# Optimization experiments

Hardware: AMD Instinct MI355X
Metric: run time of the kernel (lower is better)

Reference implementation:

```python
import jax, jax.numpy as jnp
import numpy as np

D_MODEL = 768
NUM_HEADS = 12
D_K = D_MODEL // NUM_HEADS


def setup_inputs() -> dict:
    key = jax.random.key(0)
    ks = jax.random.split(key, 12)
    B, S = 4, 2048
    s = 1.0 / np.sqrt(D_MODEL)
    inp = {
        "query": jax.random.normal(ks[0], (B, S, D_MODEL), jnp.float32),
        "key": jax.random.normal(ks[1], (B, S, D_MODEL), jnp.float32),
        "value": jax.random.normal(ks[2], (B, S, D_MODEL), jnp.float32),
        "Wq": jax.random.normal(ks[3], (D_MODEL, D_MODEL), jnp.float32) * s,
        "bq": jnp.zeros((D_MODEL,), jnp.float32),
        "Wk": jax.random.normal(ks[4], (D_MODEL, D_MODEL), jnp.float32) * s,
        "bk": jnp.zeros((D_MODEL,), jnp.float32),
        "Wv": jax.random.normal(ks[5], (D_MODEL, D_MODEL), jnp.float32) * s,
        "bv": jnp.zeros((D_MODEL,), jnp.float32),
        "Wo": jax.random.normal(ks[6], (D_MODEL, D_MODEL), jnp.float32) * s,
        "bo": jnp.zeros((D_MODEL,), jnp.float32),
    }
    return inp


def _split_heads(x):
    B, S, _ = x.shape
    return x.reshape(B, S, NUM_HEADS, D_K).transpose(0, 2, 1, 3)  # [B,H,S,Dk]


def reference(query, key, value, Wq, bq, Wk, bk, Wv, bv, Wo, bo):
    # Linear projections (torch nn.Linear: x @ W.T + b)
    Q = _split_heads(query @ Wq.T + bq)
    K = _split_heads(key @ Wk.T + bk)
    V = _split_heads(value @ Wv.T + bv)
    scale = 1.0 / jnp.sqrt(jnp.asarray(D_K, Q.dtype))
    scores = jnp.einsum("bhqd,bhkd->bhqk", Q, K) * scale  # [B,H,S,S]
    attn = jax.nn.softmax(scores, axis=-1)
    # dropout is identity in eval mode
    out = jnp.einsum("bhqk,bhkd->bhqd", attn, V)  # [B,H,S,Dk]
    B, H, S, Dk = out.shape
    out = out.transpose(0, 2, 1, 3).reshape(B, S, H * Dk)
    return out @ Wo.T + bo
```

## Files before the change

### kernel.cpp

```cpp
#include <hip/hip_runtime.h>
#include <hip/hip_bf16.h>

typedef _Float16 half8 __attribute__((ext_vector_type(8)));
typedef _Float16 h4 __attribute__((ext_vector_type(4)));
typedef __fp16 fp16x2 __attribute__((ext_vector_type(2)));
typedef float f32x4 __attribute__((ext_vector_type(4)));

#define D_MODEL 768
#define NUM_HEADS 12
#define D_K 64
#define SEQ 2048
#define BATCH 4
#define M_TOTAL (BATCH * SEQ)
#define W_ELEMS (D_MODEL * D_MODEL)
#define X_ELEMS (M_TOTAL * D_MODEL)
#define QSCALE 0.18033688011112042f
#define SOFF 4.0f

__device__ __forceinline__ void gll16(const _Float16* g, _Float16* l) {
    __builtin_amdgcn_global_load_lds(
        (const __attribute__((address_space(1))) unsigned int*)g,
        (__attribute__((address_space(3))) unsigned int*)l,
        16, 0, 0);
}

__device__ __forceinline__ void pk2(float a, float b, _Float16* out) {
    fp16x2 r = __builtin_amdgcn_cvt_pkrtz(a, b);
    out[0] = (_Float16)r[0];
    out[1] = (_Float16)r[1];
}

__global__ void convert_all(
    const float* __restrict__ w0, const float* __restrict__ w1,
    const float* __restrict__ w2, const float* __restrict__ w3,
    const float* __restrict__ x0, const float* __restrict__ x1,
    const float* __restrict__ x2, _Float16* __restrict__ dst)
{
    const size_t W4 = W_ELEMS / 4, X4 = X_ELEMS / 4;
    size_t i = (size_t)blockIdx.x * blockDim.x + threadIdx.x;
    const float* src;
    size_t off;
    if (i < 4 * W4) {
        size_t slab = i / W4;
        off = i - slab * W4;
        src = (slab == 0) ? w0 : (slab == 1) ? w1 : (slab == 2) ? w2 : w3;
    } else {
        size_t j = i - 4 * W4;
        size_t slab = j / X4;
        off = j - slab * X4;
        src = (slab == 0) ? x0 : (slab == 1) ? x1 : x2;
    }
    float4 f = ((const float4*)src)[off];
    h4 h;
    h[0] = (_Float16)f.x; h[1] = (_Float16)f.y;
    h[2] = (_Float16)f.z; h[3] = (_Float16)f.w;
    ((h4*)dst)[i] = h;
}

__global__ __launch_bounds__(256) void gemm_qkv(
    const _Float16* __restrict__ Xall, const _Float16* __restrict__ Wall,
    const float* __restrict__ bq, const float* __restrict__ bk, const float* __restrict__ bv,
    _Float16* __restrict__ Qo, _Float16* __restrict__ Ko, _Float16* __restrict__ Vto)
{
    __shared__ __align__(16) char smem[36864];
    _Float16* As = (_Float16*)smem;
    _Float16* Bs = As + 128 * 64;

    const int z = blockIdx.z;
    const _Float16* X = Xall + (size_t)z * X_ELEMS;
    const _Float16* W = Wall + (size_t)z * W_ELEMS;

    const int t = threadIdx.x;
    const int w = t >> 6;
    const int l = t & 63;
    const int ln = t & 15;
    const int quad = (t >> 4) & 3;
    const int wm = w >> 1, wn = w & 1;
    const int m0 = blockIdx.x * 128, n0 = blockIdx.y * 128;

    const int srow = l >> 3;
    const int scol = (l & 7) ^ srow;

    f32x4 acc[4][4] = {};

    for (int k0 = 0; k0 < D_MODEL; k0 += 64) {
#pragma unroll
        for (int jj = 0; jj < 4; ++jj) {
            int j = w * 4 + jj;
            int row = j * 8 + srow;
            gll16(X + (size_t)(m0 + row) * D_MODEL + k0 + scol * 8, As + j * 512);
            gll16(W + (size_t)(n0 + row) * D_MODEL + k0 + scol * 8, Bs + j * 512);
        }
        __syncthreads();

#pragma unroll
        for (int kk = 0; kk < 2; ++kk) {
            half8 a[4], b[4];
#pragma unroll
            for (int i = 0; i < 4; ++i) {
                int ra = wm * 64 + i * 16 + ln;
                int rb = wn * 64 + i * 16 + ln;
                a[i] = *(const half8*)&As[ra * 64 + (((kk * 4 + quad) ^ (ln & 7)) * 8)];
                b[i] = *(const half8*)&Bs[rb * 64 + (((kk * 4 + quad) ^ (ln & 7)) * 8)];
            }
            if (z <= 1) {
#pragma unroll
                for (int i = 0; i < 4; ++i)
#pragma unroll
                    for (int j2 = 0; j2 < 4; ++j2)
                        acc[i][j2] = __builtin_amdgcn_mfma_f32_16x16x32_f16(b[j2], a[i], acc[i][j2], 0, 0, 0);
            } else {
#pragma unroll
                for (int i = 0; i < 4; ++i)
#pragma unroll
                    for (int j2 = 0; j2 < 4; ++j2)
                        acc[i][j2] = __builtin_amdgcn_mfma_f32_16x16x32_f16(a[i], b[j2], acc[i][j2], 0, 0, 0);
            }
        }
        __syncthreads();
    }

    if (z <= 1) {
        const float* bias = (z == 0) ? bq : bk;
        _Float16* dst = (z == 0) ? Qo : Ko;
        const int head = (n0 + wn * 64) >> 6;
#pragma unroll
        for (int i = 0; i < 4; ++i) {
            int m = m0 + wm * 64 + i * 16 + ln;
            int b_ = m >> 11, s_ = m & 2047;
            _Float16* rowp = dst + ((size_t)((b_ * NUM_HEADS + head) * SEQ + s_)) * D_K;
#pragma unroll
            for (int j = 0; j < 4; ++j) {
                int dbase = j * 16 + quad * 4;
                f32x4 bn = *(const f32x4*)&bias[n0 + wn * 64 + dbase];
                h4 o;
#pragma unroll
                for (int r = 0; r < 4; ++r) {
                    float v = acc[i][j][r] + bn[r];
                    if (z == 0) v *= QSCALE;
                    o[r] = (_Float16)v;
                }
                *(h4*)&rowp[dbase] = o;
            }
        }
    } else {
        const float* bias = bv;
        _Float16* T = (_Float16*)smem + (size_t)w * (64 * 72);
#pragma unroll
        for (int i = 0; i < 4; ++i) {
#pragma unroll
            for (int j = 0; j < 4; ++j) {
                float bn = bias[n0 + wn * 64 + j * 16 + ln];
                h4 hh;
#pragma unroll
                for (int r = 0; r < 4; ++r) hh[r] = (_Float16)(acc[i][j][r] + bn);
                *(h4*)&T[(j * 16 + ln) * 72 + i * 16 + quad * 4] = hh;
            }
        }
        const int b_ = m0 >> 11;
        const int s0 = (m0 & 2047) + wm * 64;
        const int head = (n0 >> 6) + wn;
        _Float16* base = Vto + (size_t)(b_ * NUM_HEADS + head) * D_K * SEQ + s0;
#pragma unroll
        for (int r8 = 0; r8 < 8; ++r8) {
            int nl = r8 * 8 + (l >> 3);
            half8 v = *(const half8*)&T[nl * 72 + (l & 7) * 8];
            *(half8*)(base + (size_t)nl * SEQ + (l & 7) * 8) = v;
        }
    }
}

__global__ __launch_bounds__(256) void attn(
    const _Float16* __restrict__ Qg, const _Float16* __restrict__ Kg,
    const _Float16* __restrict__ Vtg, _Float16* __restrict__ ctx)
{
    __shared__ __align__(16) _Float16 Ks[2][64 * 64];
    __shared__ __align__(16) _Float16 Vs[2][64 * 64];

    const int t = threadIdx.x;
    const int w = t >> 6;
    const int l = t & 63;
    const int ln = t & 15;
    const int quad = (t >> 4) & 3;

    const int lid = blockIdx.x + (int)gridDim.x * blockIdx.y;
    const int nid = (lid & 7) * ((SEQ / 128) * (BATCH * NUM_HEADS) / 8) + (lid >> 3);
    const int bh = nid >> 4;
    const int q0 = (nid & 15) * 128 + w * 32;

    const _Float16* Qh = Qg + (size_t)bh * SEQ * D_K;
    const _Float16* Kh = Kg + (size_t)bh * SEQ * D_K;
    const _Float16* Vh = Vtg + (size_t)bh * D_K * SEQ;

    const int srow = l >> 3;
    const int scol = (l & 7) ^ srow;
    const int j0 = w * 2, j1 = w * 2 + 1;
    const _Float16* Ksrc0 = Kh + (size_t)(j0 * 8 + srow) * D_K + scol * 8;
    const _Float16* Ksrc1 = Kh + (size_t)(j1 * 8 + srow) * D_K + scol * 8;
    const _Float16* Vsrc0 = Vh + (size_t)(j0 * 8 + srow) * SEQ + scol * 8;
    const _Float16* Vsrc1 = Vh + (size_t)(j1 * 8 + srow) * SEQ + scol * 8;

    half8 qf[2][2];
#pragma unroll
    for (int qt = 0; qt < 2; ++qt)
#pragma unroll
        for (int dh = 0; dh < 2; ++dh)
            qf[qt][dh] = *(const half8*)(Qh + (size_t)(q0 + qt * 16 + ln) * D_K + dh * 32 + quad * 8);

    f32x4 acc[2][4] = {};
    f32x4 lsum[2] = {};

    gll16(Ksrc0, &Ks[0][j0 * 512]);
    gll16(Ksrc1, &Ks[0][j1 * 512]);
    gll16(Vsrc0, &Vs[0][j0 * 512]);
    gll16(Vsrc1, &Vs[0][j1 * 512]);
    asm volatile("s_waitcnt vmcnt(0)" ::: "memory");
    __builtin_amdgcn_s_barrier();

    int cur = 0;
    for (int c = 0; c < SEQ / 64; ++c) {
        if (c + 1 < SEQ / 64) {
            const size_t koff = (size_t)(c + 1) * 64 * D_K;
            const size_t voff = (size_t)(c + 1) * 64;
            gll16(Ksrc0 + koff, &Ks[cur ^ 1][j0 * 512]);
            gll16(Ksrc1 + koff, &Ks[cur ^ 1][j1 * 512]);
            gll16(Vsrc0 + voff, &Vs[cur ^ 1][j0 * 512]);
            gll16(Vsrc1 + voff, &Vs[cur ^ 1][j1 * 512]);
        }

        const _Float16* Ksc = Ks[cur];
        const _Float16* Vsc = Vs[cur];

        h4 vfr[4][4];
#pragma unroll
        for (int dt = 0; dt < 4; ++dt)
#pragma unroll
            for (int kt = 0; kt < 4; ++kt) {
                int g = kt * 2 + (quad >> 1);
                vfr[dt][kt] = *(const h4*)&Vsc[(dt * 16 + ln) * 64 + ((g ^ (ln & 7)) * 8) + (quad & 1) * 4];
            }

        h4 pB[2][4];
#pragma unroll
        for (int kt = 0; kt < 4; ++kt) {
            half8 kf0 = *(const half8*)&Ksc[(kt * 16 + ln) * 64 + ((quad ^ (ln & 7)) * 8)];
            half8 kf1 = *(const half8*)&Ksc[(kt * 16 + ln) * 64 + (((4 + quad) ^ (ln & 7)) * 8)];
#pragma unroll
            for (int qt = 0; qt < 2; ++qt) {
                f32x4 s = {-SOFF, -SOFF, -SOFF, -SOFF};
                s = __builtin_amdgcn_mfma_f32_16x16x32_f16(kf0, qf[qt][0], s, 0, 0, 0);
                s = __builtin_amdgcn_mfma_f32_16x16x32_f16(kf1, qf[qt][1], s, 0, 0, 0);
                f32x4 p;
                p[0] = __builtin_amdgcn_exp2f(s[0]);
                p[1] = __builtin_amdgcn_exp2f(s[1]);
                p[2] = __builtin_amdgcn_exp2f(s[2]);
                p[3] = __builtin_amdgcn_exp2f(s[3]);
                lsum[qt] += p;
                h4 h;
                pk2(p[0], p[1], (_Float16*)&h);
                pk2(p[2], p[3], ((_Float16*)&h) + 2);
                pB[qt][kt] = h;
            }
        }

#pragma unroll
        for (int dt = 0; dt < 4; ++dt)
#pragma unroll
            for (int kt = 0; kt < 4; ++kt) {
                acc[0][dt] = __builtin_amdgcn_mfma_f32_16x16x16f16(vfr[dt][kt], pB[0][kt], acc[0][dt], 0, 0, 0);
                acc[1][dt] = __builtin_amdgcn_mfma_f32_16x16x16f16(vfr[dt][kt], pB[1][kt], acc[1][dt], 0, 0, 0);
            }

        asm volatile("s_waitcnt vmcnt(0)" ::: "memory");
        __builtin_amdgcn_s_barrier();
        cur ^= 1;
    }

    const int h = bh % NUM_HEADS, b = bh / NUM_HEADS;
#pragma unroll
    for (int qt = 0; qt < 2; ++qt) {
        float lp = lsum[qt][0] + lsum[qt][1] + lsum[qt][2] + lsum[qt][3];
        lp += __shfl_xor(lp, 16);
        lp += __shfl_xor(lp, 32);
        float rinv = __builtin_amdgcn_rcpf(lp);
        int q = q0 + qt * 16 + ln;
#pragma unroll
        for (int dt = 0; dt < 4; ++dt) {
            h4 o;
            o[0] = (_Float16)(acc[qt][dt][0] * rinv);
            o[1] = (_Float16)(acc[qt][dt][1] * rinv);
            o[2] = (_Float16)(acc[qt][dt][2] * rinv);
            o[3] = (_Float16)(acc[qt][dt][3] * rinv);
            *(h4*)&ctx[((size_t)(b * SEQ + q)) * D_MODEL + h * D_K + dt * 16 + quad * 4] = o;
        }
    }
}

__global__ __launch_bounds__(256) void gemm_out(
    const _Float16* __restrict__ A, const _Float16* __restrict__ W,
    const float* __restrict__ bo, float* __restrict__ out)
{
    __shared__ __align__(16) _Float16 As[128 * 64];
    __shared__ __align__(16) _Float16 Bs[128 * 64];

    const int t = threadIdx.x;
    const int w = t >> 6;
    const int l = t & 63;
    const int ln = t & 15;
    const int quad = (t >> 4) & 3;
    const int wm = w >> 1, wn = w & 1;
    const int m0 = blockIdx.x * 128, n0 = blockIdx.y * 128;

    const int srow = l >> 3;
    const int scol = (l & 7) ^ srow;

    f32x4 acc[4][4] = {};

    for (int k0 = 0; k0 < D_MODEL; k0 += 64) {
#pragma unroll
        for (int jj = 0; jj < 4; ++jj) {
            int j = w * 4 + jj;
            int row = j * 8 + srow;
            gll16(A + (size_t)(m0 + row) * D_MODEL + k0 + scol * 8, As + j * 512);
            gll16(W + (size_t)(n0 + row) * D_MODEL + k0 + scol * 8, Bs + j * 512);
        }
        __syncthreads();

#pragma unroll
        for (int kk = 0; kk < 2; ++kk) {
            half8 a[4], b[4];
#pragma unroll
            for (int i = 0; i < 4; ++i) {
                int ra = wm * 64 + i * 16 + ln;
                int rb = wn * 64 + i * 16 + ln;
                a[i] = *(const half8*)&As[ra * 64 + (((kk * 4 + quad) ^ (ln & 7)) * 8)];
                b[i] = *(const half8*)&Bs[rb * 64 + (((kk * 4 + quad) ^ (ln & 7)) * 8)];
            }
#pragma unroll
            for (int i = 0; i < 4; ++i)
#pragma unroll
                for (int j2 = 0; j2 < 4; ++j2)
                    acc[i][j2] = __builtin_amdgcn_mfma_f32_16x16x32_f16(b[j2], a[i], acc[i][j2], 0, 0, 0);
        }
        __syncthreads();
    }

#pragma unroll
    for (int i = 0; i < 4; ++i) {
        int m = m0 + wm * 64 + i * 16 + ln;
        float* rowp = out + (size_t)m * D_MODEL;
#pragma unroll
        for (int j = 0; j < 4; ++j) {
            int nb = n0 + wn * 64 + j * 16 + quad * 4;
            f32x4 o = acc[i][j] + *(const f32x4*)&bo[nb];
            *(f32x4*)&rowp[nb] = o;
        }
    }
}

extern "C" void kernel_launch(void* const* d_in, const int* in_sizes, int n_in,
                              void* d_out, int out_size, void* d_ws, size_t ws_size,
                              hipStream_t stream) {
    const float* query = (const float*)d_in[0];
    const float* key   = (const float*)d_in[1];
    const float* value = (const float*)d_in[2];
    const float* Wq = (const float*)d_in[3];
    const float* bq = (const float*)d_in[4];
    const float* Wk = (const float*)d_in[5];
    const float* bk = (const float*)d_in[6];
    const float* Wv = (const float*)d_in[7];
    const float* bv = (const float*)d_in[8];
    const float* Wo = (const float*)d_in[9];
    const float* bo = (const float*)d_in[10];
    float* out = (float*)d_out;

    _Float16* ws = (_Float16*)d_ws;
    _Float16* Wb  = ws;
    _Float16* Xb  = Wb + 4 * (size_t)W_ELEMS;
    _Float16* Qb  = Xb + 3 * (size_t)X_ELEMS;
    _Float16* Kb  = Qb + (size_t)X_ELEMS;
    _Float16* Vtb = Kb + (size_t)X_ELEMS;
    _Float16* ctx = Vtb + (size_t)X_ELEMS;

    const size_t total4 = (4 * (size_t)W_ELEMS + 3 * (size_t)X_ELEMS) / 4;
    convert_all<<<(int)(total4 / 256), 256, 0, stream>>>(
        Wq, Wk, Wv, Wo, query, key, value, Wb);

    gemm_qkv<<<dim3(M_TOTAL / 128, D_MODEL / 128, 3), 256, 0, stream>>>(
        Xb, Wb, bq, bk, bv, Qb, Kb, Vtb);

    attn<<<dim3(SEQ / 128, BATCH * NUM_HEADS), 256, 0, stream>>>(Qb, Kb, Vtb, ctx);

    gemm_out<<<dim3(M_TOTAL / 128, D_MODEL / 128), 256, 0, stream>>>(
        ctx, Wb + 3 * (size_t)W_ELEMS, bo, out);
}
```

Before: 283.9 us.

## Split attention work across 8 waves with 16 query rows each

The attention block grows from 4 to 8 waves (512 threads), and each wave now owns 16 query rows instead of 32, which halves the per-wave Q fragments, accumulators and P tiles. Each wave loads one 8-row slice of the K/V tiles instead of two, so the cooperative load is spread over twice as many waves. V fragments are now loaded per dt inside the PV loop rather than all up front, and that loop raises wave priority with s_setprio. The aim is lower register pressure, higher occupancy and better latency hiding. In exchange, every wave reads K and V from LDS for only 16 rows, which doubles LDS read traffic per output, and there are more waves per barrier.

```diff
diff --git a/kernel.cpp b/kernel.cpp
--- a/kernel.cpp
+++ b/kernel.cpp
@@ -170,7 +170,7 @@
     }
 }
 
-__global__ __launch_bounds__(256) void attn(
+__global__ __launch_bounds__(512, 6) void attn(
     const _Float16* __restrict__ Qg, const _Float16* __restrict__ Kg,
     const _Float16* __restrict__ Vtg, _Float16* __restrict__ ctx)
 {
@@ -186,7 +186,7 @@
     const int lid = blockIdx.x + (int)gridDim.x * blockIdx.y;
     const int nid = (lid & 7) * ((SEQ / 128) * (BATCH * NUM_HEADS) / 8) + (lid >> 3);
     const int bh = nid >> 4;
-    const int q0 = (nid & 15) * 128 + w * 32;
+    const int q0 = (nid & 15) * 128 + w * 16;
 
     const _Float16* Qh = Qg + (size_t)bh * SEQ * D_K;
     const _Float16* Kh = Kg + (size_t)bh * SEQ * D_K;
@@ -194,82 +194,66 @@
 
     const int srow = l >> 3;
     const int scol = (l & 7) ^ srow;
-    const int j0 = w * 2, j1 = w * 2 + 1;
-    const _Float16* Ksrc0 = Kh + (size_t)(j0 * 8 + srow) * D_K + scol * 8;
-    const _Float16* Ksrc1 = Kh + (size_t)(j1 * 8 + srow) * D_K + scol * 8;
-    const _Float16* Vsrc0 = Vh + (size_t)(j0 * 8 + srow) * SEQ + scol * 8;
-    const _Float16* Vsrc1 = Vh + (size_t)(j1 * 8 + srow) * SEQ + scol * 8;
-
-    half8 qf[2][2];
-#pragma unroll
-    for (int qt = 0; qt < 2; ++qt)
-#pragma unroll
-        for (int dh = 0; dh < 2; ++dh)
-            qf[qt][dh] = *(const half8*)(Qh + (size_t)(q0 + qt * 16 + ln) * D_K + dh * 32 + quad * 8);
-
-    f32x4 acc[2][4] = {};
-    f32x4 lsum[2] = {};
-
-    gll16(Ksrc0, &Ks[0][j0 * 512]);
-    gll16(Ksrc1, &Ks[0][j1 * 512]);
-    gll16(Vsrc0, &Vs[0][j0 * 512]);
-    gll16(Vsrc1, &Vs[0][j1 * 512]);
+    const _Float16* Ksrc = Kh + (size_t)(w * 8 + srow) * D_K + scol * 8;
+    const _Float16* Vsrc = Vh + (size_t)(w * 8 + srow) * SEQ + scol * 8;
+
+    half8 qf[2];
+#pragma unroll
+    for (int dh = 0; dh < 2; ++dh)
+        qf[dh] = *(const half8*)(Qh + (size_t)(q0 + ln) * D_K + dh * 32 + quad * 8);
+
+    f32x4 acc[4] = {};
+    f32x4 lsum = {};
+
+    gll16(Ksrc, &Ks[0][w * 512]);
+    gll16(Vsrc, &Vs[0][w * 512]);
     asm volatile("s_waitcnt vmcnt(0)" ::: "memory");
     __builtin_amdgcn_s_barrier();
 
     int cur = 0;
     for (int c = 0; c < SEQ / 64; ++c) {
         if (c + 1 < SEQ / 64) {
-            const size_t koff = (size_t)(c + 1) * 64 * D_K;
-            const size_t voff = (size_t)(c + 1) * 64;
-            gll16(Ksrc0 + koff, &Ks[cur ^ 1][j0 * 512]);
-            gll16(Ksrc1 + koff, &Ks[cur ^ 1][j1 * 512]);
-            gll16(Vsrc0 + voff, &Vs[cur ^ 1][j0 * 512]);
-            gll16(Vsrc1 + voff, &Vs[cur ^ 1][j1 * 512]);
+            gll16(Ksrc + (size_t)(c + 1) * 64 * D_K, &Ks[cur ^ 1][w * 512]);
+            gll16(Vsrc + (size_t)(c + 1) * 64, &Vs[cur ^ 1][w * 512]);
         }
 
         const _Float16* Ksc = Ks[cur];
         const _Float16* Vsc = Vs[cur];
 
-        h4 vfr[4][4];
-#pragma unroll
-        for (int dt = 0; dt < 4; ++dt)
-#pragma unroll
-            for (int kt = 0; kt < 4; ++kt) {
-                int g = kt * 2 + (quad >> 1);
-                vfr[dt][kt] = *(const h4*)&Vsc[(dt * 16 + ln) * 64 + ((g ^ (ln & 7)) * 8) + (quad & 1) * 4];
-            }
-
-        h4 pB[2][4];
+        h4 pB[4];
 #pragma unroll
         for (int kt = 0; kt < 4; ++kt) {
             half8 kf0 = *(const half8*)&Ksc[(kt * 16 + ln) * 64 + ((quad ^ (ln & 7)) * 8)];
             half8 kf1 = *(const half8*)&Ksc[(kt * 16 + ln) * 64 + (((4 + quad) ^ (ln & 7)) * 8)];
-#pragma unroll
-            for (int qt = 0; qt < 2; ++qt) {
-                f32x4 s = {-SOFF, -SOFF, -SOFF, -SOFF};
-                s = __builtin_amdgcn_mfma_f32_16x16x32_f16(kf0, qf[qt][0], s, 0, 0, 0);
-                s = __builtin_amdgcn_mfma_f32_16x16x32_f16(kf1, qf[qt][1], s, 0, 0, 0);
-                f32x4 p;
-                p[0] = __builtin_amdgcn_exp2f(s[0]);
-                p[1] = __builtin_amdgcn_exp2f(s[1]);
-                p[2] = __builtin_amdgcn_exp2f(s[2]);
-                p[3] = __builtin_amdgcn_exp2f(s[3]);
-                lsum[qt] += p;
-                h4 h;
-                pk2(p[0], p[1], (_Float16*)&h);
-                pk2(p[2], p[3], ((_Float16*)&h) + 2);
-                pB[qt][kt] = h;
-            }
-        }
-
-#pragma unroll
-        for (int dt = 0; dt < 4; ++dt)
+            f32x4 s = {-SOFF, -SOFF, -SOFF, -SOFF};
+            s = __builtin_amdgcn_mfma_f32_16x16x32_f16(kf0, qf[0], s, 0, 0, 0);
+            s = __builtin_amdgcn_mfma_f32_16x16x32_f16(kf1, qf[1], s, 0, 0, 0);
+            f32x4 p;
+            p[0] = __builtin_amdgcn_exp2f(s[0]);
+            p[1] = __builtin_amdgcn_exp2f(s[1]);
+            p[2] = __builtin_amdgcn_exp2f(s[2]);
+            p[3] = __builtin_amdgcn_exp2f(s[3]);
+            lsum += p;
+            h4 h;
+            pk2(p[0], p[1], (_Float16*)&h);
+            pk2(p[2], p[3], ((_Float16*)&h) + 2);
+            pB[kt] = h;
+        }
+
+        __builtin_amdgcn_s_setprio(1);
+#pragma unroll
+        for (int dt = 0; dt < 4; ++dt) {
+            h4 vfr[4];
 #pragma unroll
             for (int kt = 0; kt < 4; ++kt) {
-                acc[0][dt] = __builtin_amdgcn_mfma_f32_16x16x16f16(vfr[dt][kt], pB[0][kt], acc[0][dt], 0, 0, 0);
-                acc[1][dt] = __builtin_amdgcn_mfma_f32_16x16x16f16(vfr[dt][kt], pB[1][kt], acc[1][dt], 0, 0, 0);
-            }
+                int g = kt * 2 + (quad >> 1);
+                vfr[kt] = *(const h4*)&Vsc[(dt * 16 + ln) * 64 + ((g ^ (ln & 7)) * 8) + (quad & 1) * 4];
+            }
+#pragma unroll
+            for (int kt = 0; kt < 4; ++kt)
+                acc[dt] = __builtin_amdgcn_mfma_f32_16x16x16f16(vfr[kt], pB[kt], acc[dt], 0, 0, 0);
+        }
+        __builtin_amdgcn_s_setprio(0);
 
         asm volatile("s_waitcnt vmcnt(0)" ::: "memory");
         __builtin_amdgcn_s_barrier();
@@ -277,20 +261,19 @@
     }
 
     const int h = bh % NUM_HEADS, b = bh / NUM_HEADS;
-#pragma unroll
-    for (int qt = 0; qt < 2; ++qt) {
-        float lp = lsum[qt][0] + lsum[qt][1] + lsum[qt][2] + lsum[qt][3];
+    {
+        float lp = lsum[0] + lsum[1] + lsum[2] + lsum[3];
         lp += __shfl_xor(lp, 16);
         lp += __shfl_xor(lp, 32);
         float rinv = __builtin_amdgcn_rcpf(lp);
-        int q = q0 + qt * 16 + ln;
+        int q = q0 + ln;
 #pragma unroll
         for (int dt = 0; dt < 4; ++dt) {
             h4 o;
-            o[0] = (_Float16)(acc[qt][dt][0] * rinv);
-            o[1] = (_Float16)(acc[qt][dt][1] * rinv);
-            o[2] = (_Float16)(acc[qt][dt][2] * rinv);
-            o[3] = (_Float16)(acc[qt][dt][3] * rinv);
+            o[0] = (_Float16)(acc[dt][0] * rinv);
+            o[1] = (_Float16)(acc[dt][1] * rinv);
+            o[2] = (_Float16)(acc[dt][2] * rinv);
+            o[3] = (_Float16)(acc[dt][3] * rinv);
             *(h4*)&ctx[((size_t)(b * SEQ + q)) * D_MODEL + h * D_K + dt * 16 + quad * 4] = o;
         }
     }
@@ -389,7 +372,7 @@
     gemm_qkv<<<dim3(M_TOTAL / 128, D_MODEL / 128, 3), 256, 0, stream>>>(
         Xb, Wb, bq, bk, bv, Qb, Kb, Vtb);
 
-    attn<<<dim3(SEQ / 128, BATCH * NUM_HEADS), 256, 0, stream>>>(Qb, Kb, Vtb, ctx);
+    attn<<<dim3(SEQ / 128, BATCH * NUM_HEADS), 512, 0, stream>>>(Qb, Kb, Vtb, ctx);
 
     gemm_out<<<dim3(M_TOTAL / 128, D_MODEL / 128), 256, 0, stream>>>(
         ctx, Wb + 3 * (size_t)W_ELEMS, bo, out);
```

After: 273.4 us. -3.7%, faster.
